# Kernel tuning notes

Hardware: AMD Instinct MI355X
Metric: run time of the kernel (lower is better)

Reference implementation:

```python
import jax, jax.numpy as jnp
import numpy as np

N = 100000      # nodes
E = 3200000     # edges (avg degree 32)
F_IN = 32       # n_features
H = 64          # GCN hidden width


def setup_inputs() -> dict:
    key = jax.random.key(0)
    ks = jax.random.split(key, 14)
    x = jax.random.normal(ks[0], (N, F_IN), jnp.float32)
    edge_index = jax.random.randint(ks[1], (2, E), 0, N, dtype=jnp.int32)
    labels = jax.random.bernoulli(ks[2], 0.1, (N, 1)).astype(jnp.float32)

    def lin(k, fan_in, fan_out):
        kw, kb = jax.random.split(k)
        bound = 1.0 / np.sqrt(fan_in)
        W = jax.random.uniform(kw, (fan_in, fan_out), jnp.float32, -bound, bound)
        b = jax.random.uniform(kb, (fan_out,), jnp.float32, -bound, bound)
        return W, b

    W1, b1 = lin(ks[3], F_IN, H)
    W2, b2 = lin(ks[4], H, H)
    W3, b3 = lin(ks[5], H, H)
    Wl1, bl1 = lin(ks[6], H, 8)
    Wl2, bl2 = lin(ks[7], 8, 1)
    return dict(x=x, edge_index=edge_index, labels=labels,
                W1=W1, b1=b1, W2=W2, b2=b2, W3=W3, b3=b3,
                Wl1=Wl1, bl1=bl1, Wl2=Wl2, bl2=bl2)


def _gcn(h, row, col, norm_edge, deg_inv, W, b):
    # GCNConv: D^{-1/2} (A + I) D^{-1/2} (h W) + b, with added self-loops.
    m = h @ W                                   # [N, out]
    msg = m[row] * norm_edge[:, None]           # [E, out] gather + scale
    agg = jax.ops.segment_sum(msg, col, num_segments=N)
    agg = agg + m * deg_inv[:, None]            # self-loop term: deg^{-1/2}_i * deg^{-1/2}_i
    return agg + b


def reference(x, edge_index, labels, W1, b1, W2, b2, W3, b3, Wl1, bl1, Wl2, bl2):
    row, col = edge_index[0], edge_index[1]
    # degree with self-loops (counts incoming edges at target nodes)
    deg = jax.ops.segment_sum(jnp.ones((E,), jnp.float32), col, num_segments=N) + 1.0
    deg_isqrt = jax.lax.rsqrt(deg)
    norm_edge = deg_isqrt[row] * deg_isqrt[col]  # [E]
    deg_inv = deg_isqrt * deg_isqrt              # self-loop norm = 1/deg

    h = jax.nn.relu(_gcn(x, row, col, norm_edge, deg_inv, W1, b1))
    # dropout is identity in eval mode
    h = jax.nn.relu(_gcn(h, row, col, norm_edge, deg_inv, W2, b2))
    h = jax.nn.relu(_gcn(h, row, col, norm_edge, deg_inv, W3, b3))
    h = jax.nn.relu(h @ Wl1 + bl1)
    z = h @ Wl2 + bl2                            # [N, 1]
    p = jax.nn.sigmoid(z)

    # generate_weights(labels): class-balanced weights
    n_pos = jnp.sum(labels)
    n_tot = jnp.float32(labels.size)
    w_pos = n_tot / (2.0 * n_pos)
    w_neg = n_tot / (2.0 * (n_tot - n_pos))
    w = labels * w_pos + (1.0 - labels) * w_neg

    # stable BCE on logits (equivalent to binary_cross_entropy(sigmoid(z), y))
    bce = -(labels * jax.nn.log_sigmoid(z) + (1.0 - labels) * jax.nn.log_sigmoid(-z))
    loss = jnp.mean(w * bce)
    return (loss, p)
```

## Files before the change

kernel.cpp:

```cpp
#include <hip/hip_runtime.h>
#include <math.h>

#define N_NODES 100000
#define N_EDGES 3200000
#define NPB 256
#define NBUCK ((N_NODES + NPB - 1) / NPB)
#define NPW 4

typedef unsigned short ushort_t;

static __device__ __forceinline__ float bf2f(ushort_t u) {
    return __uint_as_float(((unsigned int)u) << 16);
}
static __device__ __forceinline__ unsigned int f2bf_u(float f) {
    unsigned int x = __float_as_uint(f);
    unsigned int lsb = (x >> 16) & 1u;
    x += 0x7fffu + lsb;
    return x >> 16;
}
static __device__ __forceinline__ ushort_t f2bf(float f) { return (ushort_t)f2bf_u(f); }

__global__ void bucket_hist_kernel(const int* __restrict__ col, int* __restrict__ bucketCnt) {
    __shared__ int h[NBUCK];
    for (int t = threadIdx.x; t < NBUCK; t += 256) h[t] = 0;
    __syncthreads();
    for (int e = blockIdx.x * 256 + threadIdx.x; e < N_EDGES; e += gridDim.x * 256)
        atomicAdd(&h[col[e] >> 8], 1);
    __syncthreads();
    for (int t = threadIdx.x; t < NBUCK; t += 256)
        if (h[t]) atomicAdd(&bucketCnt[t], h[t]);
}

__global__ void bucket_scan_kernel(const int* __restrict__ bucketCnt, int* __restrict__ bucketOff,
                                   int* __restrict__ bcursor) {
    __shared__ int tmp[512];
    int tx = threadIdx.x;
    int v = (tx < NBUCK) ? bucketCnt[tx] : 0;
    tmp[tx] = v;
    __syncthreads();
    for (int off = 1; off < 512; off <<= 1) {
        int t = (tx >= off) ? tmp[tx - off] : 0;
        __syncthreads();
        if (tx >= off) tmp[tx] += t;
        __syncthreads();
    }
    if (tx < NBUCK) {
        int o = tmp[tx] - v;
        bucketOff[tx] = o;
        bcursor[tx] = o;
    }
}

__global__ void bin_kernel(const int* __restrict__ row, const int* __restrict__ col,
                           int* __restrict__ bcursor, int2* __restrict__ tmpE) {
    __shared__ int hist[NBUCK];
    __shared__ int chunkOff[NBUCK];
    int tx = threadIdx.x;
    for (int t = tx; t < NBUCK; t += 512) hist[t] = 0;
    __syncthreads();
    int base = blockIdx.x * 4096;
    int myc[8], myr[8], myrank[8];
#pragma unroll 8
    for (int k = 0; k < 8; ++k) {
        int idx = base + k * 512 + tx;
        bool valid = idx < N_EDGES;
        int c = valid ? col[idx] : 0;
        int r = valid ? row[idx] : 0;
        myc[k] = c;
        myr[k] = r;
        myrank[k] = valid ? atomicAdd(&hist[c >> 8], 1) : 0;
    }
    __syncthreads();
    for (int t = tx; t < NBUCK; t += 512) {
        int hv = hist[t];
        chunkOff[t] = hv ? atomicAdd(&bcursor[t], hv) : 0;
    }
    __syncthreads();
#pragma unroll 8
    for (int k = 0; k < 8; ++k) {
        int idx = base + k * 512 + tx;
        if (idx < N_EDGES) {
            int pos = chunkOff[myc[k] >> 8] + myrank[k];
            tmpE[pos] = make_int2(myr[k], myc[k]);
        }
    }
}

__global__ void csr_kernel(const int2* __restrict__ tmpE, const int* __restrict__ bucketOff,
                           const int* __restrict__ bucketCnt, int* __restrict__ starts,
                           int* __restrict__ edgeRow, float* __restrict__ isq,
                           const float* __restrict__ labels, float* __restrict__ npos) {
    __shared__ int scnt[NPB];
    __shared__ int sscan[NPB];
    __shared__ int scur[NPB];
    __shared__ float red[NPB];
    int b = blockIdx.x;
    int lo = b * NPB;
    int nn = N_NODES - lo;
    if (nn > NPB) nn = NPB;
    int base = bucketOff[b];
    int ecnt = bucketCnt[b];
    int tx = threadIdx.x;
    scnt[tx] = 0;
    __syncthreads();
    for (int t = tx; t < ecnt; t += NPB) atomicAdd(&scnt[tmpE[base + t].y - lo], 1);
    __syncthreads();
    int v = scnt[tx];
    sscan[tx] = v;
    __syncthreads();
    for (int off = 1; off < NPB; off <<= 1) {
        int t = (tx >= off) ? sscan[tx - off] : 0;
        __syncthreads();
        if (tx >= off) sscan[tx] += t;
        __syncthreads();
    }
    int excl = sscan[tx] - v;
    scur[tx] = excl;
    float lab = 0.0f;
    if (tx < nn) {
        starts[lo + tx] = base + excl;
        isq[lo + tx] = rsqrtf((float)v + 1.0f);
        lab = labels[lo + tx];
    }
    if (b == NBUCK - 1 && tx == 0) starts[N_NODES] = N_EDGES;
    red[tx] = lab;
    __syncthreads();
    for (int s = NPB / 2; s > 0; s >>= 1) {
        if (tx < s) red[tx] += red[tx + s];
        __syncthreads();
    }
    if (tx == 0) atomicAdd(npos, red[0]);
    for (int t = tx; t < ecnt; t += NPB) {
        int2 rc = tmpE[base + t];
        int p = atomicAdd(&scur[rc.y - lo], 1);
        edgeRow[base + p] = rc.x;
    }
}

__global__ void xcast_kernel(const float* __restrict__ x, const float* __restrict__ isq,
                             ushort_t* __restrict__ xs) {
    int i = blockIdx.x * 256 + threadIdx.x;
    if (i < (N_NODES * 32) / 4) {
        float s = isq[i >> 3];
        float4 v = ((const float4*)x)[i];
        ushort4 o;
        o.x = f2bf(v.x * s); o.y = f2bf(v.y * s); o.z = f2bf(v.z * s); o.w = f2bf(v.w * s);
        ((ushort4*)xs)[i] = o;
    }
}

__global__ void wpack_kernel(const float* __restrict__ W1, const float* __restrict__ W2,
                             const float* __restrict__ W3, unsigned int* __restrict__ wp) {
    int t = blockIdx.x * 256 + threadIdx.x;
    if (t >= 80 * 64) return;
    int k2 = t >> 6, l = t & 63;
    const float* W;
    int kk;
    if (k2 < 16) { W = W1; kk = k2; }
    else if (k2 < 48) { W = W2; kk = k2 - 16; }
    else { W = W3; kk = k2 - 48; }
    float lo = W[(2 * kk) * 64 + l];
    float hi = W[(2 * kk + 1) * 64 + l];
    wp[t] = (f2bf_u(hi) << 16) | f2bf_u(lo);
}

__global__ void fused32_kernel(const int* __restrict__ starts, const int* __restrict__ edgeRow,
                               const ushort_t* __restrict__ xs, const float* __restrict__ isq,
                               const unsigned int* __restrict__ wpG,
                               const float* __restrict__ bias, ushort_t* __restrict__ hout) {
    __shared__ float sAgg[4][32];
    int w = threadIdx.x >> 6;
    int lane = threadIdx.x & 63;
    int f = lane & 31, half = lane >> 5;
    unsigned int wpk[16];
#pragma unroll
    for (int k2 = 0; k2 < 16; ++k2) wpk[k2] = wpG[k2 * 64 + lane];
    float bias_r = bias[lane];
    int nodeBase = blockIdx.x * (4 * NPW) + w * NPW;
    for (int i = 0; i < NPW; ++i) {
        int node = __builtin_amdgcn_readfirstlane(nodeBase + i);
        int sU = starts[node];
        int eU = starts[node + 1];
        float sic = isq[node];
        float acc[4] = {0.0f, 0.0f, 0.0f, 0.0f};
        int ngrp = (eU - sU + 15) >> 4;
        int jb = sU;
        for (int g = 0; g < ngrp; ++g) {
            int rows[16];
#pragma unroll
            for (int q = 0; q < 16; ++q) rows[q] = edgeRow[jb + q];
            unsigned int vv[16];
#pragma unroll
            for (int q = 0; q < 16; ++q) vv[q] = xs[(rows[q] << 5) + f];
#pragma unroll
            for (int q = 0; q < 16; ++q) {
                float n = (jb + q < eU) ? 1.0f : 0.0f;
                acc[q & 3] = fmaf(bf2f((ushort_t)vv[q]), n, acc[q & 3]);
            }
            jb += 16;
        }
        float accsum = (acc[0] + acc[1]) + (acc[2] + acc[3]);
        if (half == 0) {
            accsum += bf2f(xs[(node << 5) + f]);
            sAgg[w][f] = accsum * sic;
        }
        float o = bias_r;
#pragma unroll
        for (int q = 0; q < 8; ++q) {
            float4 av = *(const float4*)&sAgg[w][q * 4];
            unsigned int p0 = wpk[2 * q], p1 = wpk[2 * q + 1];
            o = fmaf(av.x, __uint_as_float(p0 << 16), o);
            o = fmaf(av.y, __uint_as_float(p0 & 0xffff0000u), o);
            o = fmaf(av.z, __uint_as_float(p1 << 16), o);
            o = fmaf(av.w, __uint_as_float(p1 & 0xffff0000u), o);
        }
        o = o > 0.0f ? o : 0.0f;
        hout[(node << 6) + lane] = f2bf(o * sic);
    }
}

__global__ void fused64_kernel(const int* __restrict__ starts, const int* __restrict__ edgeRow,
                               const ushort_t* __restrict__ hs, const float* __restrict__ isq,
                               const unsigned int* __restrict__ wpG,
                               const float* __restrict__ bias, ushort_t* __restrict__ hout,
                               int outScaled) {
    __shared__ float sAgg[4][64];
    int w = threadIdx.x >> 6;
    int lane = threadIdx.x & 63;
    unsigned int wpk[32];
#pragma unroll
    for (int k2 = 0; k2 < 32; ++k2) wpk[k2] = wpG[k2 * 64 + lane];
    float bias_r = bias[lane];
    int nodeBase = blockIdx.x * (4 * NPW) + w * NPW;
    for (int i = 0; i < NPW; ++i) {
        int node = __builtin_amdgcn_readfirstlane(nodeBase + i);
        int sU = starts[node];
        int eU = starts[node + 1];
        float sic = isq[node];
        float acc[4];
        acc[0] = bf2f(hs[(node << 6) + lane]);
        acc[1] = 0.0f; acc[2] = 0.0f; acc[3] = 0.0f;
        int ngrp = (eU - sU + 15) >> 4;
        int jb = sU;
        for (int g = 0; g < ngrp; ++g) {
            int rows[16];
#pragma unroll
            for (int q = 0; q < 16; ++q) rows[q] = edgeRow[jb + q];
            unsigned int vv[16];
#pragma unroll
            for (int q = 0; q < 16; ++q) vv[q] = hs[(rows[q] << 6) + lane];
#pragma unroll
            for (int q = 0; q < 16; ++q) {
                float n = (jb + q < eU) ? 1.0f : 0.0f;
                acc[q & 3] = fmaf(bf2f((ushort_t)vv[q]), n, acc[q & 3]);
            }
            jb += 16;
        }
        sAgg[w][lane] = ((acc[0] + acc[1]) + (acc[2] + acc[3])) * sic;
        float o = bias_r;
#pragma unroll
        for (int q = 0; q < 16; ++q) {
            float4 av = *(const float4*)&sAgg[w][q * 4];
            unsigned int p0 = wpk[2 * q], p1 = wpk[2 * q + 1];
            o = fmaf(av.x, __uint_as_float(p0 << 16), o);
            o = fmaf(av.y, __uint_as_float(p0 & 0xffff0000u), o);
            o = fmaf(av.z, __uint_as_float(p1 << 16), o);
            o = fmaf(av.w, __uint_as_float(p1 & 0xffff0000u), o);
        }
        o = o > 0.0f ? o : 0.0f;
        float scale = outScaled ? sic : 1.0f;
        hout[(node << 6) + lane] = f2bf(o * scale);
    }
}

__global__ void head_kernel(const ushort_t* __restrict__ h, const float* __restrict__ Wl1,
                            const float* __restrict__ bl1, const float* __restrict__ Wl2,
                            const float* __restrict__ bl2, const float* __restrict__ labels,
                            const float* __restrict__ npos, float* __restrict__ out) {
    __shared__ float sW1[64 * 8];
    __shared__ float sb1[8];
    __shared__ float sW2[8];
    for (int t = threadIdx.x; t < 512; t += 256) sW1[t] = Wl1[t];
    if (threadIdx.x < 8) {
        sb1[threadIdx.x] = bl1[threadIdx.x];
        sW2[threadIdx.x] = Wl2[threadIdx.x];
    }
    __syncthreads();
    int i = blockIdx.x * 256 + threadIdx.x;
    float contrib = 0.0f;
    if (i < N_NODES) {
        const ushort4* hr4 = (const ushort4*)(h + (size_t)i * 64);
        float a[8];
#pragma unroll
        for (int j = 0; j < 8; ++j) a[j] = sb1[j];
#pragma unroll
        for (int kb = 0; kb < 16; ++kb) {
            ushort4 v4 = hr4[kb];
            float h0 = bf2f(v4.x), h1 = bf2f(v4.y), h2 = bf2f(v4.z), h3 = bf2f(v4.w);
#pragma unroll
            for (int j = 0; j < 8; ++j) {
                a[j] = fmaf(h0, sW1[(kb * 4 + 0) * 8 + j], a[j]);
                a[j] = fmaf(h1, sW1[(kb * 4 + 1) * 8 + j], a[j]);
                a[j] = fmaf(h2, sW1[(kb * 4 + 2) * 8 + j], a[j]);
                a[j] = fmaf(h3, sW1[(kb * 4 + 3) * 8 + j], a[j]);
            }
        }
        float z = bl2[0];
#pragma unroll
        for (int j = 0; j < 8; ++j) {
            float r = a[j] > 0.0f ? a[j] : 0.0f;
            z = fmaf(r, sW2[j], z);
        }
        float p = 1.0f / (1.0f + expf(-z));
        out[1 + i] = p;
        float y = labels[i];
        float np = *npos;
        float fn = (float)N_NODES;
        float wpos = fn / (2.0f * np);
        float wneg = fn / (2.0f * (fn - np));
        float wgt = y * wpos + (1.0f - y) * wneg;
        float lse = log1pf(expf(-fabsf(z)));
        float ls_pos = fminf(z, 0.0f) - lse;
        float ls_neg = fminf(-z, 0.0f) - lse;
        float bce = -(y * ls_pos + (1.0f - y) * ls_neg);
        contrib = wgt * bce / fn;
    }
    __shared__ float red[256];
    red[threadIdx.x] = contrib;
    __syncthreads();
    for (int s = 128; s > 0; s >>= 1) {
        if (threadIdx.x < s) red[threadIdx.x] += red[threadIdx.x + s];
        __syncthreads();
    }
    if (threadIdx.x == 0) atomicAdd(out, red[0]);
}

extern "C" void kernel_launch(void* const* d_in, const int* in_sizes, int n_in,
                              void* d_out, int out_size, void* d_ws, size_t ws_size,
                              hipStream_t stream) {
    const float* x      = (const float*)d_in[0];
    const int*   ei     = (const int*)d_in[1];
    const float* labels = (const float*)d_in[2];
    const float* W1  = (const float*)d_in[3];
    const float* b1  = (const float*)d_in[4];
    const float* W2  = (const float*)d_in[5];
    const float* b2  = (const float*)d_in[6];
    const float* W3  = (const float*)d_in[7];
    const float* b3  = (const float*)d_in[8];
    const float* Wl1 = (const float*)d_in[9];
    const float* bl1 = (const float*)d_in[10];
    const float* Wl2 = (const float*)d_in[11];
    const float* bl2 = (const float*)d_in[12];

    const int* row = ei;
    const int* col = ei + N_EDGES;
    float* out = (float*)d_out;

    char* w = (char*)d_ws;
    int2*     tmpE    = (int2*)w;
    int*      edgeRow = (int*)(w + (size_t)N_EDGES * 8);
    ushort_t* xbf     = (ushort_t*)(edgeRow + N_EDGES + 16);
    ushort_t* hbfA    = xbf + (size_t)N_NODES * 32;
    ushort_t* hbfB    = hbfA + (size_t)N_NODES * 64;
    int*      starts  = (int*)(hbfB + (size_t)N_NODES * 64);
    int*      bucketCnt = starts + (N_NODES + 1);
    int*      bucketOff = bucketCnt + NBUCK;
    int*      bcursor   = bucketOff + NBUCK;
    float*    isq  = (float*)(bcursor + NBUCK);
    float*    npos = isq + N_NODES;
    unsigned int* wpG = (unsigned int*)(npos + 1);

    hipMemsetAsync(bucketCnt, 0, NBUCK * sizeof(int), stream);
    hipMemsetAsync(npos, 0, sizeof(float), stream);
    hipMemsetAsync(out, 0, sizeof(float), stream);
    hipMemsetAsync(edgeRow + N_EDGES, 0, 16 * sizeof(int), stream);

    const int FB = N_NODES / (4 * NPW);
    const int BB = (N_EDGES + 4095) / 4096;
    const int XB = (N_NODES * 32 / 4 + 255) / 256;

    bucket_hist_kernel<<<1024, 256, 0, stream>>>(col, bucketCnt);
    bucket_scan_kernel<<<1, 512, 0, stream>>>(bucketCnt, bucketOff, bcursor);
    bin_kernel<<<BB, 512, 0, stream>>>(row, col, bcursor, tmpE);
    csr_kernel<<<NBUCK, NPB, 0, stream>>>(tmpE, bucketOff, bucketCnt, starts, edgeRow, isq,
                                          labels, npos);
    xcast_kernel<<<XB, 256, 0, stream>>>(x, isq, xbf);
    wpack_kernel<<<20, 256, 0, stream>>>(W1, W2, W3, wpG);

    fused32_kernel<<<FB, 256, 0, stream>>>(starts, edgeRow, xbf, isq, wpG, b1, hbfA);
    fused64_kernel<<<FB, 256, 0, stream>>>(starts, edgeRow, hbfA, isq, wpG + 16 * 64, b2,
                                           hbfB, 1);
    fused64_kernel<<<FB, 256, 0, stream>>>(starts, edgeRow, hbfB, isq, wpG + 48 * 64, b3,
                                           hbfA, 0);

    head_kernel<<<(N_NODES + 255) / 256, 256, 0, stream>>>(hbfA, Wl1, bl1, Wl2, bl2, labels,
                                                           npos, out);
}
```

Measured before the change: 415.3 us.

## Split 64-wide aggregation into four 16-feature slab passes with separate GEMM

Layer outputs are now stored as four feature slabs of 16 bf16 values per node, each 3.2 MB. Each 64-wide GCN layer is aggregated in four passes, one per slab, so the gathered table is small enough to stay cache-resident. Each pass handles four edges per wavefront step and writes fp32 partial aggregates to a buffer. A separate GEMM kernel then applies the weights, bias and ReLU. The cost is four times the edge-index reads, eight extra launches, and an fp32 aggregate buffer round trip through memory in place of the fused in-register matmul.

```diff
diff --git a/kernel.cpp b/kernel.cpp
--- a/kernel.cpp
+++ b/kernel.cpp
@@ -167,7 +167,7 @@
 __global__ void fused32_kernel(const int* __restrict__ starts, const int* __restrict__ edgeRow,
                                const ushort_t* __restrict__ xs, const float* __restrict__ isq,
                                const unsigned int* __restrict__ wpG,
-                               const float* __restrict__ bias, ushort_t* __restrict__ hout) {
+                               const float* __restrict__ bias, ushort_t* __restrict__ hsl) {
     __shared__ float sAgg[4][32];
     int w = threadIdx.x >> 6;
     int lane = threadIdx.x & 63;
@@ -215,48 +215,69 @@
             o = fmaf(av.w, __uint_as_float(p1 & 0xffff0000u), o);
         }
         o = o > 0.0f ? o : 0.0f;
-        hout[(node << 6) + lane] = f2bf(o * sic);
-    }
-}
-
-__global__ void fused64_kernel(const int* __restrict__ starts, const int* __restrict__ edgeRow,
-                               const ushort_t* __restrict__ hs, const float* __restrict__ isq,
-                               const unsigned int* __restrict__ wpG,
-                               const float* __restrict__ bias, ushort_t* __restrict__ hout,
-                               int outScaled) {
-    __shared__ float sAgg[4][64];
-    int w = threadIdx.x >> 6;
-    int lane = threadIdx.x & 63;
-    unsigned int wpk[32];
-#pragma unroll
-    for (int k2 = 0; k2 < 32; ++k2) wpk[k2] = wpG[k2 * 64 + lane];
-    float bias_r = bias[lane];
+        hsl[((lane >> 4) * N_NODES + node) * 16 + (lane & 15)] = f2bf(o * sic);
+    }
+}
+
+__global__ void agg16_kernel(const int* __restrict__ starts, const int* __restrict__ edgeRow,
+                             const ushort_t* __restrict__ slab, const float* __restrict__ isq,
+                             float* __restrict__ aggOut, int foff) {
+    int tid = threadIdx.x;
+    int w = tid >> 6;
+    int lane = tid & 63;
+    int j = lane & 15;
+    int lq = lane >> 4;
+    bool q1 = (lane & 16) != 0;
+    bool q2 = (lane & 32) != 0;
     int nodeBase = blockIdx.x * (4 * NPW) + w * NPW;
     for (int i = 0; i < NPW; ++i) {
         int node = __builtin_amdgcn_readfirstlane(nodeBase + i);
         int sU = starts[node];
         int eU = starts[node + 1];
         float sic = isq[node];
-        float acc[4];
-        acc[0] = bf2f(hs[(node << 6) + lane]);
-        acc[1] = 0.0f; acc[2] = 0.0f; acc[3] = 0.0f;
+        float acc = 0.0f, acc2 = 0.0f;
         int ngrp = (eU - sU + 15) >> 4;
         int jb = sU;
         for (int g = 0; g < ngrp; ++g) {
             int rows[16];
 #pragma unroll
             for (int q = 0; q < 16; ++q) rows[q] = edgeRow[jb + q];
-            unsigned int vv[16];
-#pragma unroll
-            for (int q = 0; q < 16; ++q) vv[q] = hs[(rows[q] << 6) + lane];
-#pragma unroll
-            for (int q = 0; q < 16; ++q) {
-                float n = (jb + q < eU) ? 1.0f : 0.0f;
-                acc[q & 3] = fmaf(bf2f((ushort_t)vv[q]), n, acc[q & 3]);
+#pragma unroll
+            for (int b = 0; b < 4; ++b) {
+                int r01 = q1 ? rows[4 * b + 1] : rows[4 * b + 0];
+                int r23 = q1 ? rows[4 * b + 3] : rows[4 * b + 2];
+                int r = q2 ? r23 : r01;
+                int eidx = jb + 4 * b + lq;
+                float nv = (eidx < eU) ? 1.0f : 0.0f;
+                float v = bf2f(slab[(r << 4) + j]);
+                if (b & 1) acc2 = fmaf(v, nv, acc2);
+                else       acc  = fmaf(v, nv, acc);
             }
             jb += 16;
         }
-        sAgg[w][lane] = ((acc[0] + acc[1]) + (acc[2] + acc[3])) * sic;
+        acc += acc2;
+        acc += __shfl_xor(acc, 16);
+        acc += __shfl_xor(acc, 32);
+        acc += bf2f(slab[(node << 4) + j]);
+        acc *= sic;
+        if (lane < 16) aggOut[(node << 6) + foff + j] = acc;
+    }
+}
+
+__global__ void gemm64_kernel(const float* __restrict__ agg, const unsigned int* __restrict__ wpG,
+                              const float* __restrict__ bias, const float* __restrict__ isq,
+                              ushort_t* __restrict__ outp, int sliced) {
+    __shared__ float sAgg[4][64];
+    int w = threadIdx.x >> 6;
+    int lane = threadIdx.x & 63;
+    unsigned int wpk[32];
+#pragma unroll
+    for (int k2 = 0; k2 < 32; ++k2) wpk[k2] = wpG[(k2 << 6) + lane];
+    float bias_r = bias[lane];
+    int nodeBase = blockIdx.x * (4 * NPW) + w * NPW;
+    for (int i = 0; i < NPW; ++i) {
+        int node = nodeBase + i;
+        sAgg[w][lane] = agg[(node << 6) + lane];
         float o = bias_r;
 #pragma unroll
         for (int q = 0; q < 16; ++q) {
@@ -268,8 +289,11 @@
             o = fmaf(av.w, __uint_as_float(p1 & 0xffff0000u), o);
         }
         o = o > 0.0f ? o : 0.0f;
-        float scale = outScaled ? sic : 1.0f;
-        hout[(node << 6) + lane] = f2bf(o * scale);
+        if (sliced) {
+            outp[((lane >> 4) * N_NODES + node) * 16 + (lane & 15)] = f2bf(o * isq[node]);
+        } else {
+            outp[(node << 6) + lane] = f2bf(o);
+        }
     }
 }
 
@@ -358,11 +382,13 @@
 
     char* w = (char*)d_ws;
     int2*     tmpE    = (int2*)w;
+    float*    aggBuf  = (float*)w;
     int*      edgeRow = (int*)(w + (size_t)N_EDGES * 8);
-    ushort_t* xbf     = (ushort_t*)(edgeRow + N_EDGES + 16);
-    ushort_t* hbfA    = xbf + (size_t)N_NODES * 32;
-    ushort_t* hbfB    = hbfA + (size_t)N_NODES * 64;
-    int*      starts  = (int*)(hbfB + (size_t)N_NODES * 64);
+    ushort_t* xs      = (ushort_t*)(edgeRow + N_EDGES + 16);
+    ushort_t* hsl1    = xs + (size_t)N_NODES * 32;
+    ushort_t* hsl2    = hsl1 + (size_t)N_NODES * 64;
+    ushort_t* hbfF    = hsl2 + (size_t)N_NODES * 64;
+    int*      starts  = (int*)(hbfF + (size_t)N_NODES * 64);
     int*      bucketCnt = starts + (N_NODES + 1);
     int*      bucketOff = bucketCnt + NBUCK;
     int*      bcursor   = bucketOff + NBUCK;
@@ -378,21 +404,28 @@
     const int FB = N_NODES / (4 * NPW);
     const int BB = (N_EDGES + 4095) / 4096;
     const int XB = (N_NODES * 32 / 4 + 255) / 256;
+    const int SLAB = N_NODES * 16;
 
     bucket_hist_kernel<<<1024, 256, 0, stream>>>(col, bucketCnt);
     bucket_scan_kernel<<<1, 512, 0, stream>>>(bucketCnt, bucketOff, bcursor);
     bin_kernel<<<BB, 512, 0, stream>>>(row, col, bcursor, tmpE);
     csr_kernel<<<NBUCK, NPB, 0, stream>>>(tmpE, bucketOff, bucketCnt, starts, edgeRow, isq,
                                           labels, npos);
-    xcast_kernel<<<XB, 256, 0, stream>>>(x, isq, xbf);
+    xcast_kernel<<<XB, 256, 0, stream>>>(x, isq, xs);
     wpack_kernel<<<20, 256, 0, stream>>>(W1, W2, W3, wpG);
 
-    fused32_kernel<<<FB, 256, 0, stream>>>(starts, edgeRow, xbf, isq, wpG, b1, hbfA);
-    fused64_kernel<<<FB, 256, 0, stream>>>(starts, edgeRow, hbfA, isq, wpG + 16 * 64, b2,
-                                           hbfB, 1);
-    fused64_kernel<<<FB, 256, 0, stream>>>(starts, edgeRow, hbfB, isq, wpG + 48 * 64, b3,
-                                           hbfA, 0);
-
-    head_kernel<<<(N_NODES + 255) / 256, 256, 0, stream>>>(hbfA, Wl1, bl1, Wl2, bl2, labels,
+    fused32_kernel<<<FB, 256, 0, stream>>>(starts, edgeRow, xs, isq, wpG, b1, hsl1);
+
+    for (int p = 0; p < 4; ++p)
+        agg16_kernel<<<FB, 256, 0, stream>>>(starts, edgeRow, hsl1 + (size_t)p * SLAB, isq,
+                                             aggBuf, p * 16);
+    gemm64_kernel<<<FB, 256, 0, stream>>>(aggBuf, wpG + 16 * 64, b2, isq, hsl2, 1);
+
+    for (int p = 0; p < 4; ++p)
+        agg16_kernel<<<FB, 256, 0, stream>>>(starts, edgeRow, hsl2 + (size_t)p * SLAB, isq,
+                                             aggBuf, p * 16);
+    gemm64_kernel<<<FB, 256, 0, stream>>>(aggBuf, wpG + 48 * 64, b3, isq, hbfF, 0);
+
+    head_kernel<<<(N_NODES + 255) / 256, 256, 0, stream>>>(hbfF, Wl1, bl1, Wl2, bl2, labels,
                                                            npos, out);
 }
```

Result: slower. 1.538 ms (+270.4%).

## Pack binned edges into 32-bit words and sub-sort CSR rows by source segment

Applied to the files above, without the earlier changes.

The bucket-binning pass now stores each edge as one 32-bit word holding the 17-bit source row and the 8-bit local target, replacing an int2. This halves the temporary edge buffer traffic. The CSR builder counts per (target, source-range) segment, so each node's neighbour list is roughly sorted by source index, which should improve gather locality in the later aggregation kernels. The cost is an 8x larger shared histogram and extra per-thread scan work.

```diff
diff --git a/kernel.cpp b/kernel.cpp
--- a/kernel.cpp
+++ b/kernel.cpp
@@ -6,6 +6,7 @@
 #define NPB 256
 #define NBUCK ((N_NODES + NPB - 1) / NPB)
 #define NPW 4
+#define NSEG 8
 
 typedef unsigned short ushort_t;
 
@@ -52,7 +53,7 @@
 }
 
 __global__ void bin_kernel(const int* __restrict__ row, const int* __restrict__ col,
-                           int* __restrict__ bcursor, int2* __restrict__ tmpE) {
+                           int* __restrict__ bcursor, unsigned int* __restrict__ tmpE) {
     __shared__ int hist[NBUCK];
     __shared__ int chunkOff[NBUCK];
     int tx = threadIdx.x;
@@ -81,18 +82,17 @@
         int idx = base + k * 512 + tx;
         if (idx < N_EDGES) {
             int pos = chunkOff[myc[k] >> 8] + myrank[k];
-            tmpE[pos] = make_int2(myr[k], myc[k]);
-        }
-    }
-}
-
-__global__ void csr_kernel(const int2* __restrict__ tmpE, const int* __restrict__ bucketOff,
+            tmpE[pos] = (unsigned int)myr[k] | ((unsigned int)(myc[k] & 255) << 17);
+        }
+    }
+}
+
+__global__ void csr_kernel(const unsigned int* __restrict__ tmpE, const int* __restrict__ bucketOff,
                            const int* __restrict__ bucketCnt, int* __restrict__ starts,
                            int* __restrict__ edgeRow, float* __restrict__ isq,
                            const float* __restrict__ labels, float* __restrict__ npos) {
-    __shared__ int scnt[NPB];
-    __shared__ int sscan[NPB];
-    __shared__ int scur[NPB];
+    __shared__ int scnt[NPB * NSEG];
+    __shared__ int tsum[NPB];
     __shared__ float red[NPB];
     int b = blockIdx.x;
     int lo = b * NPB;
@@ -101,25 +101,42 @@
     int base = bucketOff[b];
     int ecnt = bucketCnt[b];
     int tx = threadIdx.x;
-    scnt[tx] = 0;
-    __syncthreads();
-    for (int t = tx; t < ecnt; t += NPB) atomicAdd(&scnt[tmpE[base + t].y - lo], 1);
-    __syncthreads();
-    int v = scnt[tx];
-    sscan[tx] = v;
-    __syncthreads();
+    for (int t = tx; t < NPB * NSEG; t += NPB) scnt[t] = 0;
+    __syncthreads();
+    for (int t = tx; t < ecnt; t += NPB) {
+        unsigned int v = tmpE[base + t];
+        int r = v & 0x1FFFF;
+        int cl = v >> 17;
+        atomicAdd(&scnt[cl * NSEG + (r >> 14)], 1);
+    }
+    __syncthreads();
+    int my[NSEG];
+    int deg = 0;
+#pragma unroll
+    for (int s = 0; s < NSEG; ++s) {
+        my[s] = scnt[tx * NSEG + s];
+        deg += my[s];
+    }
+    tsum[tx] = deg;
+    __syncthreads();
+    int v = tsum[tx];
     for (int off = 1; off < NPB; off <<= 1) {
-        int t = (tx >= off) ? sscan[tx - off] : 0;
-        __syncthreads();
-        if (tx >= off) sscan[tx] += t;
-        __syncthreads();
-    }
-    int excl = sscan[tx] - v;
-    scur[tx] = excl;
+        int t = (tx >= off) ? tsum[tx - off] : 0;
+        __syncthreads();
+        if (tx >= off) tsum[tx] += t;
+        __syncthreads();
+    }
+    int nodeOff = tsum[tx] - v;
+    int run = nodeOff;
+#pragma unroll
+    for (int s = 0; s < NSEG; ++s) {
+        scnt[tx * NSEG + s] = run;
+        run += my[s];
+    }
     float lab = 0.0f;
     if (tx < nn) {
-        starts[lo + tx] = base + excl;
-        isq[lo + tx] = rsqrtf((float)v + 1.0f);
+        starts[lo + tx] = base + nodeOff;
+        isq[lo + tx] = rsqrtf((float)deg + 1.0f);
         lab = labels[lo + tx];
     }
     if (b == NBUCK - 1 && tx == 0) starts[N_NODES] = N_EDGES;
@@ -130,10 +147,13 @@
         __syncthreads();
     }
     if (tx == 0) atomicAdd(npos, red[0]);
+    __syncthreads();
     for (int t = tx; t < ecnt; t += NPB) {
-        int2 rc = tmpE[base + t];
-        int p = atomicAdd(&scur[rc.y - lo], 1);
-        edgeRow[base + p] = rc.x;
+        unsigned int v2 = tmpE[base + t];
+        int r = v2 & 0x1FFFF;
+        int cl = v2 >> 17;
+        int p = atomicAdd(&scnt[cl * NSEG + (r >> 14)], 1);
+        edgeRow[base + p] = r;
     }
 }
 
@@ -357,8 +377,8 @@
     float* out = (float*)d_out;
 
     char* w = (char*)d_ws;
-    int2*     tmpE    = (int2*)w;
-    int*      edgeRow = (int*)(w + (size_t)N_EDGES * 8);
+    unsigned int* tmpE = (unsigned int*)w;
+    int*      edgeRow = (int*)(w + (size_t)N_EDGES * 4);
     ushort_t* xbf     = (ushort_t*)(edgeRow + N_EDGES + 16);
     ushort_t* hbfA    = xbf + (size_t)N_NODES * 32;
     ushort_t* hbfB    = hbfA + (size_t)N_NODES * 64;
```

After: 415.7 us. Within noise of the previous version (+0.1%).
